# Optimization experiments

Measured on AMD Instinct MI355X. Metric: run time of the kernel, lower is better.

## Reference

```python
import jax, jax.numpy as jnp
import numpy as np

DIM = 1024
NUM_EXPERTS = 64
TOP_K = 8


def setup_inputs() -> dict:
    key = jax.random.key(0)
    kx, kw, kb = jax.random.split(key, 3)
    x = jax.random.normal(kx, (8, 4096, DIM), dtype=jnp.float32)
    # nn.Linear(dim, num_experts): weight [E, D], bias [E]
    bound = 1.0 / np.sqrt(DIM)
    W = jax.random.uniform(kw, (NUM_EXPERTS, DIM), minval=-bound, maxval=bound, dtype=jnp.float32)
    b = jax.random.uniform(kb, (NUM_EXPERTS,), minval=-bound, maxval=bound, dtype=jnp.float32)
    return {"x": x, "W": W, "b": b}


def reference(x, W, b):
    B, S, D = x.shape
    E = W.shape[0]
    # router logits: [B, S, E]
    logits = jnp.einsum("bsd,ed->bse", x, W) + b
    # top-k per token
    top_vals, indices = jax.lax.top_k(logits, TOP_K)  # [B,S,K]
    # scatter top-k logits into -inf tensor, then softmax
    flat_logits = logits.reshape(-1, E)
    flat_idx = indices.reshape(-1, TOP_K)
    flat_vals = top_vals.reshape(-1, TOP_K)
    rows = jnp.arange(flat_logits.shape[0])[:, None]
    sparse = jnp.full_like(flat_logits, -jnp.inf).at[rows, flat_idx].set(flat_vals)
    probs = jax.nn.softmax(sparse, axis=-1).reshape(B, S, E)
    return probs, indices
```

## Files before the change

kernel.cpp:

```cpp
#include <hip/hip_runtime.h>
#include <math.h>

#define DIM 1024
#define NEXP 64
#define TOPK 8
#define BM 128
#define BK 64
#define NCHUNK (DIM / BK)
#define THREADS 256
#define LPAD 65

__device__ __forceinline__ void gload16(const float* g, float* l) {
    __builtin_amdgcn_global_load_lds(
        (const __attribute__((address_space(1))) void*)g,
        (__attribute__((address_space(3))) void*)l, 16, 0, 0);
}

__global__ __launch_bounds__(THREADS, 1)
void router_topk_kernel(const float* __restrict__ x,
                        const float* __restrict__ W,
                        const float* __restrict__ b,
                        float* __restrict__ out_probs,
                        float* __restrict__ out_idx)
{
    __shared__ float x_s[2][BM][BK];
    __shared__ float w_s[2][NEXP][BK];
    __shared__ float logits_s[BM][LPAD];
    __shared__ float topk_s[BM][TOPK];

    const int tid  = threadIdx.x;
    const int trow = tid >> 4;
    const int tcol = tid & 15;
    const int lane = tid & 63;
    const int wv   = tid >> 6;
    const int tok0 = blockIdx.x * BM;

    float bb[4];
#pragma unroll
    for (int j = 0; j < 4; ++j) bb[j] = b[tcol + 16 * j];

    float acc[8][4];
#pragma unroll
    for (int i = 0; i < 8; ++i)
#pragma unroll
        for (int j = 0; j < 4; ++j) acc[i][j] = 0.f;

    const int rl = lane >> 4;
    const int c  = lane & 15;
    auto stage = [&](int buf, int kc) {
#pragma unroll
        for (int k = 0; k < 8; ++k) {
            int r  = wv * 32 + k * 4 + rl;
            int cs = c ^ (r & 15);
            gload16(x + (size_t)(tok0 + r) * DIM + kc * BK + cs * 4,
                    &x_s[buf][r][c * 4]);
        }
#pragma unroll
        for (int k = 0; k < 4; ++k) {
            int r  = wv * 16 + k * 4 + rl;
            int cs = c ^ (r & 15);
            gload16(W + (size_t)r * DIM + kc * BK + cs * 4,
                    &w_s[buf][r][c * 4]);
        }
    };

    auto compute = [&](int buf) {
#pragma unroll
        for (int k4 = 0; k4 < 16; ++k4) {
            const int cx = (k4 ^ trow) * 4;
            const int cw = (k4 ^ tcol) * 4;
            float4 xa[8], wa[4];
#pragma unroll
            for (int i = 0; i < 8; ++i)
                xa[i] = *(const float4*)&x_s[buf][trow + 16 * i][cx];
#pragma unroll
            for (int j = 0; j < 4; ++j)
                wa[j] = *(const float4*)&w_s[buf][tcol + 16 * j][cw];
#pragma unroll
            for (int i = 0; i < 8; ++i)
#pragma unroll
                for (int j = 0; j < 4; ++j) {
                    acc[i][j] = fmaf(xa[i].x, wa[j].x, acc[i][j]);
                    acc[i][j] = fmaf(xa[i].y, wa[j].y, acc[i][j]);
                    acc[i][j] = fmaf(xa[i].z, wa[j].z, acc[i][j]);
                    acc[i][j] = fmaf(xa[i].w, wa[j].w, acc[i][j]);
                }
        }
    };

    stage(0, 0);
    __syncthreads();
    for (int kc = 0; kc < NCHUNK; ++kc) {
        const int cur = kc & 1;
        if (kc + 1 < NCHUNK) stage(cur ^ 1, kc + 1);
        compute(cur);
        __syncthreads();
    }

#pragma unroll
    for (int i = 0; i < 8; ++i)
#pragma unroll
        for (int j = 0; j < 4; ++j)
            logits_s[trow + 16 * i][tcol + 16 * j] = acc[i][j] + bb[j];
    __syncthreads();

    if (tid < BM) {
        const int t = tid;
        float pv[TOPK]; int pi[TOPK];
#pragma unroll
        for (int k = 0; k < TOPK; ++k) {
            float vmax = -INFINITY; int imax = 0;
#pragma unroll
            for (int e = 0; e < NEXP; ++e) {
                float v = logits_s[t][e];
                if (v > vmax) { vmax = v; imax = e; }
            }
            pv[k] = vmax; pi[k] = imax;
            logits_s[t][imax] = -INFINITY;
        }
        float p[TOPK]; float s = 0.f;
#pragma unroll
        for (int k = 0; k < TOPK; ++k) { p[k] = __expf(pv[k] - pv[0]); s += p[k]; }
        float inv = 1.f / s;

#pragma unroll
        for (int e = 0; e < NEXP; ++e) logits_s[t][e] = 0.f;
#pragma unroll
        for (int k = 0; k < TOPK; ++k) {
            logits_s[t][pi[k]] = p[k] * inv;
            topk_s[t][k] = (float)pi[k];
        }
    }
    __syncthreads();

#pragma unroll
    for (int i = 0; i < 8; ++i) {
        int v = tid + i * THREADS;
        int row = v >> 4, cc = (v & 15) * 4;
        float4 z = make_float4(logits_s[row][cc], logits_s[row][cc + 1],
                               logits_s[row][cc + 2], logits_s[row][cc + 3]);
        *(float4*)(out_probs + (size_t)(tok0 + row) * NEXP + cc) = z;
    }
    {
        int row = tid >> 1, c4 = tid & 1;
        float4 z = *(const float4*)&topk_s[row][c4 * 4];
        *(float4*)(out_idx + (size_t)(tok0 + row) * TOPK + c4 * 4) = z;
    }
}

extern "C" void kernel_launch(void* const* d_in, const int* in_sizes, int n_in,
                              void* d_out, int out_size, void* d_ws, size_t ws_size,
                              hipStream_t stream) {
    const float* x = (const float*)d_in[0];
    const float* W = (const float*)d_in[1];
    const float* b = (const float*)d_in[2];
    float* out = (float*)d_out;

    const int ntok = in_sizes[0] / DIM;
    float* out_probs = out;
    float* out_idx   = out + (size_t)ntok * NEXP;

    const int grid = ntok / BM;
    router_topk_kernel<<<grid, THREADS, 0, stream>>>(x, W, b, out_probs, out_idx);
}
```

Baseline: 255.5 us.

## Split the router GEMM along K into two partial kernels plus a top-k finalize kernel

The fused GEMM+top-k kernel is split into a split-K GEMM kernel that writes two partial logit tiles to workspace, followed by a finalize kernel that sums the partials, adds bias, and does top-k and softmax. The K chunk shrinks to 32 and launch bounds allow two blocks per CU. The aim is more blocks in flight to fill the CUs (256 tiles otherwise), at the cost of extra workspace traffic and a second launch.

```diff
diff --git a/kernel.cpp b/kernel.cpp
--- a/kernel.cpp
+++ b/kernel.cpp
@@ -5,8 +5,10 @@
 #define NEXP 64
 #define TOPK 8
 #define BM 128
-#define BK 64
-#define NCHUNK (DIM / BK)
+#define KSPLIT 2
+#define KHALF (DIM / KSPLIT)
+#define BK 32
+#define NCHUNK (KHALF / BK)
 #define THREADS 256
 #define LPAD 65
 
@@ -16,28 +18,21 @@
         (__attribute__((address_space(3))) void*)l, 16, 0, 0);
 }
 
-__global__ __launch_bounds__(THREADS, 1)
-void router_topk_kernel(const float* __restrict__ x,
-                        const float* __restrict__ W,
-                        const float* __restrict__ b,
-                        float* __restrict__ out_probs,
-                        float* __restrict__ out_idx)
+__global__ __launch_bounds__(THREADS, 2)
+void router_gemm_partial(const float* __restrict__ x,
+                         const float* __restrict__ W,
+                         float* __restrict__ part)
 {
     __shared__ float x_s[2][BM][BK];
     __shared__ float w_s[2][NEXP][BK];
-    __shared__ float logits_s[BM][LPAD];
-    __shared__ float topk_s[BM][TOPK];
 
     const int tid  = threadIdx.x;
     const int trow = tid >> 4;
     const int tcol = tid & 15;
-    const int lane = tid & 63;
-    const int wv   = tid >> 6;
-    const int tok0 = blockIdx.x * BM;
-
-    float bb[4];
-#pragma unroll
-    for (int j = 0; j < 4; ++j) bb[j] = b[tcol + 16 * j];
+    const int tile = blockIdx.x;
+    const int half = blockIdx.y;
+    const int tok0 = tile * BM;
+    const int k0   = half * KHALF;
 
     float acc[8][4];
 #pragma unroll
@@ -45,30 +40,30 @@
 #pragma unroll
         for (int j = 0; j < 4; ++j) acc[i][j] = 0.f;
 
-    const int rl = lane >> 4;
-    const int c  = lane & 15;
+    const int rr = tid >> 3;
+    const int c  = tid & 7;
     auto stage = [&](int buf, int kc) {
 #pragma unroll
-        for (int k = 0; k < 8; ++k) {
-            int r  = wv * 32 + k * 4 + rl;
-            int cs = c ^ (r & 15);
-            gload16(x + (size_t)(tok0 + r) * DIM + kc * BK + cs * 4,
+        for (int m = 0; m < 4; ++m) {
+            int r  = m * 32 + rr;
+            int cs = c ^ (r & 7);
+            gload16(x + (size_t)(tok0 + r) * DIM + k0 + kc * BK + cs * 4,
                     &x_s[buf][r][c * 4]);
         }
 #pragma unroll
-        for (int k = 0; k < 4; ++k) {
-            int r  = wv * 16 + k * 4 + rl;
-            int cs = c ^ (r & 15);
-            gload16(W + (size_t)r * DIM + kc * BK + cs * 4,
+        for (int m = 0; m < 2; ++m) {
+            int r  = m * 32 + rr;
+            int cs = c ^ (r & 7);
+            gload16(W + (size_t)r * DIM + k0 + kc * BK + cs * 4,
                     &w_s[buf][r][c * 4]);
         }
     };
 
     auto compute = [&](int buf) {
 #pragma unroll
-        for (int k4 = 0; k4 < 16; ++k4) {
-            const int cx = (k4 ^ trow) * 4;
-            const int cw = (k4 ^ tcol) * 4;
+        for (int k4 = 0; k4 < 8; ++k4) {
+            const int cx = (k4 ^ (trow & 7)) * 4;
+            const int cw = (k4 ^ (tcol & 7)) * 4;
             float4 xa[8], wa[4];
 #pragma unroll
             for (int i = 0; i < 8; ++i)
@@ -97,11 +92,50 @@
         __syncthreads();
     }
 
+    float* sstage = &x_s[0][0][0];
 #pragma unroll
     for (int i = 0; i < 8; ++i)
 #pragma unroll
         for (int j = 0; j < 4; ++j)
-            logits_s[trow + 16 * i][tcol + 16 * j] = acc[i][j] + bb[j];
+            sstage[(trow + 16 * i) * NEXP + tcol + 16 * j] = acc[i][j];
+    __syncthreads();
+
+    float* dst = part + ((size_t)(tile * KSPLIT + half) * BM) * NEXP;
+#pragma unroll
+    for (int it = 0; it < 8; ++it) {
+        int v = tid + it * THREADS;
+        *(float4*)(dst + v * 4) = *(const float4*)(sstage + v * 4);
+    }
+}
+
+__global__ __launch_bounds__(THREADS, 1)
+void router_topk_finalize(const float* __restrict__ part,
+                          const float* __restrict__ b,
+                          float* __restrict__ out_probs,
+                          float* __restrict__ out_idx)
+{
+    __shared__ float logits_s[BM][LPAD];
+    __shared__ float topk_s[BM][TOPK];
+
+    const int tid  = threadIdx.x;
+    const int tile = blockIdx.x;
+    const int tok0 = tile * BM;
+
+    const float* p0 = part + ((size_t)(tile * KSPLIT + 0) * BM) * NEXP;
+    const float* p1 = part + ((size_t)(tile * KSPLIT + 1) * BM) * NEXP;
+
+#pragma unroll
+    for (int it = 0; it < 8; ++it) {
+        int v = tid + it * THREADS;
+        int r = v >> 4, c4 = (v & 15) * 4;
+        float4 a = *(const float4*)(p0 + (size_t)r * NEXP + c4);
+        float4 d = *(const float4*)(p1 + (size_t)r * NEXP + c4);
+        float4 bv = *(const float4*)(b + c4);
+        logits_s[r][c4 + 0] = a.x + d.x + bv.x;
+        logits_s[r][c4 + 1] = a.y + d.y + bv.y;
+        logits_s[r][c4 + 2] = a.z + d.z + bv.z;
+        logits_s[r][c4 + 3] = a.w + d.w + bv.w;
+    }
     __syncthreads();
 
     if (tid < BM) {
@@ -134,17 +168,17 @@
     __syncthreads();
 
 #pragma unroll
-    for (int i = 0; i < 8; ++i) {
-        int v = tid + i * THREADS;
-        int row = v >> 4, cc = (v & 15) * 4;
-        float4 z = make_float4(logits_s[row][cc], logits_s[row][cc + 1],
-                               logits_s[row][cc + 2], logits_s[row][cc + 3]);
-        *(float4*)(out_probs + (size_t)(tok0 + row) * NEXP + cc) = z;
+    for (int it = 0; it < 8; ++it) {
+        int v = tid + it * THREADS;
+        int r = v >> 4, c4 = (v & 15) * 4;
+        float4 z = make_float4(logits_s[r][c4], logits_s[r][c4 + 1],
+                               logits_s[r][c4 + 2], logits_s[r][c4 + 3]);
+        *(float4*)(out_probs + (size_t)(tok0 + r) * NEXP + c4) = z;
     }
     {
-        int row = tid >> 1, c4 = tid & 1;
-        float4 z = *(const float4*)&topk_s[row][c4 * 4];
-        *(float4*)(out_idx + (size_t)(tok0 + row) * TOPK + c4 * 4) = z;
+        int r = tid >> 1, c4 = tid & 1;
+        float4 z = *(const float4*)&topk_s[r][c4 * 4];
+        *(float4*)(out_idx + (size_t)(tok0 + r) * TOPK + c4 * 4) = z;
     }
 }
 
@@ -159,7 +193,9 @@
     const int ntok = in_sizes[0] / DIM;
     float* out_probs = out;
     float* out_idx   = out + (size_t)ntok * NEXP;
-
-    const int grid = ntok / BM;
-    router_topk_kernel<<<grid, THREADS, 0, stream>>>(x, W, b, out_probs, out_idx);
-}
+    float* part      = (float*)d_ws;
+
+    const int tiles = ntok / BM;
+    router_gemm_partial<<<dim3(tiles, KSPLIT), THREADS, 0, stream>>>(x, W, part);
+    router_topk_finalize<<<tiles, THREADS, 0, stream>>>(part, b, out_probs, out_idx);
+}
```

Measured after the change: 235.2 us. -8.0%, faster.

## Use bf16x3 split MFMA for router GEMM with pre-split weights

Applied to the files above, without the earlier changes.

Replaces the FP32 FMA GEMM with bf16 MFMA instructions. Both x and W are split into three bf16 parts (hi/lo/mid), and six MFMA products are kept to stay close to FP32 accuracy. A small pre-kernel converts and swizzles W into the workspace each call. The tile changes to 32 tokens per block with 128 threads, and x is loaded straight into registers with a one-chunk prefetch instead of going through LDS. The main risk is that top-k selection could change if the emulated precision drifts enough to flip near-tied logits.

```diff
diff --git a/kernel.cpp b/kernel.cpp
--- a/kernel.cpp
+++ b/kernel.cpp
@@ -4,104 +4,149 @@
 #define DIM 1024
 #define NEXP 64
 #define TOPK 8
-#define BM 128
-#define BK 64
-#define NCHUNK (DIM / BK)
-#define THREADS 256
+#define BM 32
+#define NCH 32
+#define THREADS 128
 #define LPAD 65
-
-__device__ __forceinline__ void gload16(const float* g, float* l) {
+#define WARR 131072
+
+typedef __attribute__((ext_vector_type(8))) short short8v;
+typedef __attribute__((ext_vector_type(4))) float f32x4;
+typedef __attribute__((ext_vector_type(4))) unsigned short ushort4v;
+
+__device__ __forceinline__ unsigned short rne_bf16(float f, float& back) {
+    unsigned u = __builtin_bit_cast(unsigned, f);
+    unsigned r = (u + 0x7FFFu + ((u >> 16) & 1u)) >> 16;
+    back = __builtin_bit_cast(float, r << 16);
+    return (unsigned short)r;
+}
+
+__device__ __forceinline__ void gload16(const void* g, void* l) {
     __builtin_amdgcn_global_load_lds(
         (const __attribute__((address_space(1))) void*)g,
         (__attribute__((address_space(3))) void*)l, 16, 0, 0);
 }
 
-__global__ __launch_bounds__(THREADS, 1)
-void router_topk_kernel(const float* __restrict__ x,
-                        const float* __restrict__ W,
-                        const float* __restrict__ b,
-                        float* __restrict__ out_probs,
-                        float* __restrict__ out_idx)
+__global__ __launch_bounds__(256)
+void wconv_kernel(const float* __restrict__ W, char* __restrict__ ws) {
+    int id = blockIdx.x * 256 + threadIdx.x;
+    int kc = id >> 8, rem = id & 255, e = rem >> 2, g = rem & 3;
+    const float* src = W + (size_t)e * DIM + kc * 32 + g * 8;
+    f32x4 v0 = *(const f32x4*)src;
+    f32x4 v1 = *(const f32x4*)(src + 4);
+    float xs[8] = {v0.x, v0.y, v0.z, v0.w, v1.x, v1.y, v1.z, v1.w};
+    ushort4v h[2], l[2], m[2];
+#pragma unroll
+    for (int i = 0; i < 8; ++i) {
+        float bh, bl, bm;
+        unsigned short hh = rne_bf16(xs[i], bh);
+        float r1 = xs[i] - bh;
+        unsigned short ll = rne_bf16(r1, bl);
+        float r2 = r1 - bl;
+        unsigned short mm = rne_bf16(r2, bm);
+        h[i >> 2][i & 3] = hh; l[i >> 2][i & 3] = ll; m[i >> 2][i & 3] = mm;
+    }
+    size_t dst = (size_t)kc * 4096 + e * 64 + (size_t)(g ^ (e & 3)) * 16;
+    *(ushort4v*)(ws + 0 * WARR + dst)     = h[0];
+    *(ushort4v*)(ws + 0 * WARR + dst + 8) = h[1];
+    *(ushort4v*)(ws + 1 * WARR + dst)     = l[0];
+    *(ushort4v*)(ws + 1 * WARR + dst + 8) = l[1];
+    *(ushort4v*)(ws + 2 * WARR + dst)     = m[0];
+    *(ushort4v*)(ws + 2 * WARR + dst + 8) = m[1];
+}
+
+__global__ __launch_bounds__(THREADS, 2)
+void router_fused_kernel(const float* __restrict__ x,
+                         const char* __restrict__ ws,
+                         const float* __restrict__ b,
+                         float* __restrict__ out_probs,
+                         float* __restrict__ out_idx)
 {
-    __shared__ float x_s[2][BM][BK];
-    __shared__ float w_s[2][NEXP][BK];
+    __shared__ __align__(16) char warena[2][3][4096];
     __shared__ float logits_s[BM][LPAD];
     __shared__ float topk_s[BM][TOPK];
 
-    const int tid  = threadIdx.x;
-    const int trow = tid >> 4;
-    const int tcol = tid & 15;
-    const int lane = tid & 63;
-    const int wv   = tid >> 6;
-    const int tok0 = blockIdx.x * BM;
-
-    float bb[4];
-#pragma unroll
-    for (int j = 0; j < 4; ++j) bb[j] = b[tcol + 16 * j];
-
-    float acc[8][4];
-#pragma unroll
-    for (int i = 0; i < 8; ++i)
-#pragma unroll
-        for (int j = 0; j < 4; ++j) acc[i][j] = 0.f;
-
-    const int rl = lane >> 4;
-    const int c  = lane & 15;
-    auto stage = [&](int buf, int kc) {
-#pragma unroll
-        for (int k = 0; k < 8; ++k) {
-            int r  = wv * 32 + k * 4 + rl;
-            int cs = c ^ (r & 15);
-            gload16(x + (size_t)(tok0 + r) * DIM + kc * BK + cs * 4,
-                    &x_s[buf][r][c * 4]);
-        }
-#pragma unroll
-        for (int k = 0; k < 4; ++k) {
-            int r  = wv * 16 + k * 4 + rl;
-            int cs = c ^ (r & 15);
-            gload16(W + (size_t)r * DIM + kc * BK + cs * 4,
-                    &w_s[buf][r][c * 4]);
+    const int tid   = threadIdx.x;
+    const int lane  = tid & 63;
+    const int wv    = tid >> 6;
+    const int e_low = lane & 15;
+    const int quad  = lane >> 4;
+    const int tok0  = blockIdx.x * BM;
+
+    float bias4[4];
+#pragma unroll
+    for (int eg = 0; eg < 4; ++eg) bias4[eg] = b[eg * 16 + e_low];
+
+    const float* xrow = x + (size_t)(tok0 + wv * 16 + e_low) * DIM + quad * 8;
+
+    const int lane_woff = e_low * 64 + ((quad ^ (e_low & 3)) * 16);
+
+    const int w6 = wv * 6;
+    auto stageW = [&](int buf, int kc) {
+#pragma unroll
+        for (int i = 0; i < 6; ++i) {
+            int seg = w6 + i;
+            int a = seg >> 2, qt = seg & 3;
+            gload16(ws + (size_t)a * WARR + (size_t)kc * 4096 + qt * 1024 + lane * 16,
+                    &warena[buf][a][qt * 1024 + lane * 16]);
         }
     };
 
-    auto compute = [&](int buf) {
-#pragma unroll
-        for (int k4 = 0; k4 < 16; ++k4) {
-            const int cx = (k4 ^ trow) * 4;
-            const int cw = (k4 ^ tcol) * 4;
-            float4 xa[8], wa[4];
-#pragma unroll
-            for (int i = 0; i < 8; ++i)
-                xa[i] = *(const float4*)&x_s[buf][trow + 16 * i][cx];
-#pragma unroll
-            for (int j = 0; j < 4; ++j)
-                wa[j] = *(const float4*)&w_s[buf][tcol + 16 * j][cw];
-#pragma unroll
-            for (int i = 0; i < 8; ++i)
-#pragma unroll
-                for (int j = 0; j < 4; ++j) {
-                    acc[i][j] = fmaf(xa[i].x, wa[j].x, acc[i][j]);
-                    acc[i][j] = fmaf(xa[i].y, wa[j].y, acc[i][j]);
-                    acc[i][j] = fmaf(xa[i].z, wa[j].z, acc[i][j]);
-                    acc[i][j] = fmaf(xa[i].w, wa[j].w, acc[i][j]);
-                }
-        }
-    };
-
-    stage(0, 0);
+    f32x4 accm[4], accs[4];
+#pragma unroll
+    for (int eg = 0; eg < 4; ++eg) {
+        accm[eg] = (f32x4){0.f, 0.f, 0.f, 0.f};
+        accs[eg] = (f32x4){0.f, 0.f, 0.f, 0.f};
+    }
+
+    stageW(0, 0);
+    f32x4 cxa = *(const f32x4*)(xrow);
+    f32x4 cxb = *(const f32x4*)(xrow + 4);
     __syncthreads();
-    for (int kc = 0; kc < NCHUNK; ++kc) {
-        const int cur = kc & 1;
-        if (kc + 1 < NCHUNK) stage(cur ^ 1, kc + 1);
-        compute(cur);
+
+    f32x4 nxa, nxb;
+    for (int kc = 0; kc < NCH; ++kc) {
+        const int buf = kc & 1;
+        if (kc + 1 < NCH) {
+            stageW(buf ^ 1, kc + 1);
+            nxa = *(const f32x4*)(xrow + (kc + 1) * 32);
+            nxb = *(const f32x4*)(xrow + (kc + 1) * 32 + 4);
+        }
+        float xs[8] = {cxa.x, cxa.y, cxa.z, cxa.w, cxb.x, cxb.y, cxb.z, cxb.w};
+        short8v xh, xl, xm;
+#pragma unroll
+        for (int i = 0; i < 8; ++i) {
+            float bh, bl, bm;
+            xh[i] = (short)rne_bf16(xs[i], bh);
+            float r1 = xs[i] - bh;
+            xl[i] = (short)rne_bf16(r1, bl);
+            float r2 = r1 - bl;
+            xm[i] = (short)rne_bf16(r2, bm);
+        }
+#pragma unroll
+        for (int eg = 0; eg < 4; ++eg) {
+            const char* pg = &warena[buf][0][0] + eg * 1024 + lane_woff;
+            short8v bh = *(const short8v*)(pg);
+            short8v bl = *(const short8v*)(pg + 4096);
+            short8v bm = *(const short8v*)(pg + 8192);
+            accm[eg] = __builtin_amdgcn_mfma_f32_16x16x32_bf16(xh, bh, accm[eg], 0, 0, 0);
+            accs[eg] = __builtin_amdgcn_mfma_f32_16x16x32_bf16(xh, bl, accs[eg], 0, 0, 0);
+            accs[eg] = __builtin_amdgcn_mfma_f32_16x16x32_bf16(xl, bh, accs[eg], 0, 0, 0);
+            accs[eg] = __builtin_amdgcn_mfma_f32_16x16x32_bf16(xl, bl, accs[eg], 0, 0, 0);
+            accs[eg] = __builtin_amdgcn_mfma_f32_16x16x32_bf16(xh, bm, accs[eg], 0, 0, 0);
+            accs[eg] = __builtin_amdgcn_mfma_f32_16x16x32_bf16(xm, bh, accs[eg], 0, 0, 0);
+        }
         __syncthreads();
-    }
-
-#pragma unroll
-    for (int i = 0; i < 8; ++i)
-#pragma unroll
-        for (int j = 0; j < 4; ++j)
-            logits_s[trow + 16 * i][tcol + 16 * j] = acc[i][j] + bb[j];
+        cxa = nxa; cxb = nxb;
+    }
+
+#pragma unroll
+    for (int eg = 0; eg < 4; ++eg)
+#pragma unroll
+        for (int q = 0; q < 4; ++q) {
+            int t = wv * 16 + quad * 4 + q;
+            logits_s[t][eg * 16 + e_low] = accm[eg][q] + accs[eg][q] + bias4[eg];
+        }
     __syncthreads();
 
     if (tid < BM) {
@@ -122,7 +167,6 @@
 #pragma unroll
         for (int k = 0; k < TOPK; ++k) { p[k] = __expf(pv[k] - pv[0]); s += p[k]; }
         float inv = 1.f / s;
-
 #pragma unroll
         for (int e = 0; e < NEXP; ++e) logits_s[t][e] = 0.f;
 #pragma unroll
@@ -134,17 +178,17 @@
     __syncthreads();
 
 #pragma unroll
-    for (int i = 0; i < 8; ++i) {
-        int v = tid + i * THREADS;
-        int row = v >> 4, cc = (v & 15) * 4;
-        float4 z = make_float4(logits_s[row][cc], logits_s[row][cc + 1],
-                               logits_s[row][cc + 2], logits_s[row][cc + 3]);
-        *(float4*)(out_probs + (size_t)(tok0 + row) * NEXP + cc) = z;
-    }
-    {
-        int row = tid >> 1, c4 = tid & 1;
-        float4 z = *(const float4*)&topk_s[row][c4 * 4];
-        *(float4*)(out_idx + (size_t)(tok0 + row) * TOPK + c4 * 4) = z;
+    for (int it = 0; it < 4; ++it) {
+        int v = tid + it * THREADS;
+        int r = v >> 4, c4 = (v & 15) * 4;
+        f32x4 z = {logits_s[r][c4], logits_s[r][c4 + 1],
+                   logits_s[r][c4 + 2], logits_s[r][c4 + 3]};
+        *(f32x4*)(out_probs + (size_t)(tok0 + r) * NEXP + c4) = z;
+    }
+    if (tid < 64) {
+        int r = tid >> 1, c4 = tid & 1;
+        f32x4 z = *(const f32x4*)&topk_s[r][c4 * 4];
+        *(f32x4*)(out_idx + (size_t)(tok0 + r) * TOPK + c4 * 4) = z;
     }
 }
 
@@ -159,7 +203,8 @@
     const int ntok = in_sizes[0] / DIM;
     float* out_probs = out;
     float* out_idx   = out + (size_t)ntok * NEXP;
-
-    const int grid = ntok / BM;
-    router_topk_kernel<<<grid, THREADS, 0, stream>>>(x, W, b, out_probs, out_idx);
-}
+    char*  ws        = (char*)d_ws;
+
+    wconv_kernel<<<32, 256, 0, stream>>>(W, ws);
+    router_fused_kernel<<<ntok / BM, THREADS, 0, stream>>>(x, ws, b, out_probs, out_idx);
+}
```

New measurement: 229.3 us. 10.2% less time.
